# Optimization experiments

Measured on AMD Instinct MI355X. Metric: run time of the kernel, lower is better.

The kernel has to match this reference:

```python
import jax, jax.numpy as jnp
import numpy as np

N_IN = 16384
G = 64            # input grid resolution
K_UP = 8          # 2^3 children per voxel for kernel=2 stride=2 generative transpose conv
N_OUT = N_IN * K_UP
G2 = 2 * G        # output grid resolution
NUMS = 32768      # top-k prune budget
C = 64


def _np_coords_and_maps():
    """Build voxel coords, the 27-offset kernel map on upsampled coords, and a fake GT mask."""
    rng = np.random.default_rng(0)
    flat = rng.choice(G ** 3, size=N_IN, replace=False)
    c = np.stack(np.unravel_index(flat, (G, G, G)), axis=1).astype(np.int64)  # [N_IN,3]
    offs2 = np.stack(np.meshgrid(*([[0, 1]] * 3), indexing='ij'), -1).reshape(-1, 3)  # [8,3]
    cu = (2 * c[:, None, :] + offs2[None]).reshape(-1, 3)  # [N_OUT,3], order n*8+k
    lut = np.full(G2 ** 3, N_OUT, dtype=np.int64)
    key = (cu[:, 0] * G2 + cu[:, 1]) * G2 + cu[:, 2]
    lut[key] = np.arange(N_OUT)
    offs3 = np.stack(np.meshgrid(*([[-1, 0, 1]] * 3), indexing='ij'), -1).reshape(-1, 3)  # [27,3]
    nbr = np.empty((27, N_OUT), np.int64)
    for k, d in enumerate(offs3):
        q = cu + d
        valid = ((q >= 0) & (q < G2)).all(1)
        qk = np.where(valid, (q[:, 0] * G2 + q[:, 1]) * G2 + q[:, 2], 0)
        nbr[k] = np.where(valid, lut[qk], N_OUT)  # N_OUT = sentinel 'missing'
    gt = rng.random(N_OUT) < 0.3  # isin(out.C, ground_truth.C) membership mask
    return nbr.astype(np.int32), gt


def setup_inputs() -> dict:
    key = jax.random.key(0)
    ks = jax.random.split(key, 10)
    nbr, gt = _np_coords_and_maps()
    s = 0.05
    rn = lambda k, shape: jax.random.normal(k, shape, jnp.float32) * s
    z = lambda shape: jnp.zeros(shape, jnp.float32)
    return {
        "x_feats": jax.random.normal(ks[0], (N_IN, C), jnp.float32),
        "Wup": rn(ks[1], (K_UP, C, C)), "bup": z((C,)),
        "Wc0": rn(ks[2], (27, C, C)), "bc0": z((C,)),
        "W00": rn(ks[3], (3, 27, C, C // 4)), "b00": z((3, C // 4)),
        "W01": rn(ks[4], (3, 27, C // 4, C // 2)), "b01": z((3, C // 2)),
        "W10": rn(ks[5], (3, C, C // 4)), "b10": z((3, C // 4)),
        "W11": rn(ks[6], (3, 27, C // 4, C // 4)), "b11": z((3, C // 4)),
        "W12": rn(ks[7], (3, C // 4, C // 2)), "b12": z((3, C // 2)),
        "Wcls": rn(ks[8], (27, C, 1)), "bcls": z((1,)),
        "nbr_idx": jnp.asarray(nbr), "mask_true": jnp.asarray(gt),
        "nums": NUMS,
    }


def sparse_conv(feats, nbr, W, b):
    """Gather-GEMM-scatter sparse conv: feats [N,Cin], nbr [K,N] (N = missing), W [K,Cin,Cout]."""
    fp = jnp.concatenate([feats, jnp.zeros((1, feats.shape[1]), feats.dtype)], axis=0)
    def body(acc, wn):
        Wk, nk = wn
        return acc + fp[nk] @ Wk, None
    acc0 = jnp.zeros((feats.shape[0], W.shape[-1]), feats.dtype)
    out, _ = jax.lax.scan(body, acc0, (W, nbr))
    return out + b


def reference(x_feats, Wup, bup, Wc0, bc0, W00, b00, W01, b01, W10, b10, W11, b11, W12, b12, Wcls, bcls, nbr_idx, mask_true, nums):
    # generative transpose conv k=2 s=2: each voxel emits 8 children (no overlaps)
    up = jnp.einsum('nc,kcd->nkd', x_feats, Wup).reshape(-1, Wup.shape[-1]) + bup  # [N_OUT,C]
    out = jax.nn.relu(up)
    out = jax.nn.relu(sparse_conv(out, nbr_idx, Wc0, bc0))
    for i in range(3):  # 3 InceptionResNet blocks
        o0 = sparse_conv(jax.nn.relu(sparse_conv(out, nbr_idx, W00[i], b00[i])), nbr_idx, W01[i], b01[i])
        t = jax.nn.relu(out @ W10[i] + b10[i])            # 1x1 conv
        t = jax.nn.relu(sparse_conv(t, nbr_idx, W11[i], b11[i]))
        o1 = t @ W12[i] + b12[i]                          # 1x1 conv
        out = jnp.concatenate([o0, o1], axis=1) + out
    out_cls = sparse_conv(out, nbr_idx, Wcls, bcls)       # [N_OUT,1]
    _, idx = jax.lax.top_k(out_cls[:, 0], nums)           # istopk
    mask = jnp.zeros((out.shape[0],), bool).at[idx].set(True) | mask_true  # topk + isin(GT)
    pruned = out * mask[:, None].astype(out.dtype)        # pruning as mask (static shape)
    return out_cls, pruned, mask
```

## Files before the change

kernel.cpp:

```cpp
#include <hip/hip_runtime.h>
#include <cstdint>

#define NOUTC 131072
#define NINC  16384

using uint = unsigned int;

__device__ __forceinline__ uint fkey(float v){
  uint u = __float_as_uint(v);
  return (u & 0x80000000u) ? ~u : (u | 0x80000000u);
}

template<int ROWS, int CIN, int COUT, int TR, int TC, int NK, bool IDENT, bool RELU, bool RESID>
__global__ __launch_bounds__(256)
void spconv(const float* __restrict__ feats,
            const int*   __restrict__ nbr,
            const float* __restrict__ Wg,
            const float* __restrict__ bias,
            const float* __restrict__ resid,
            float*       __restrict__ outp,
            int ostride, int coff)
{
  static_assert(TR == 4, "TR must be 4");
  static_assert((ROWS / TR) * (COUT / TC) == 256, "thread tiling must cover 256 threads");
  constexpr int TPR = 256 / ROWS;
  static_assert(ROWS * TPR == 256, "");
  constexpr int GV = CIN / (4 * TPR);
  static_assert(CIN % (4 * TPR) == 0, "");
  constexpr int STR = ROWS + 4;

  __shared__ float Wl[CIN * COUT];
  __shared__ float ft[CIN][STR];

  const int t    = threadIdx.x;
  const int base = blockIdx.x * ROWS;

  constexpr int CT = COUT / TC;
  const int tcc = (t % CT) * TC;
  const int trr = (t / CT) * TR;

  const int gr    = t / TPR;
  const int gpart = t % TPR;

  float acc[TR][TC];
  #pragma unroll
  for (int a = 0; a < TR; ++a)
    #pragma unroll
    for (int b = 0; b < TC; ++b) acc[a][b] = 0.f;

  for (int k = 0; k < NK; ++k) {
    #pragma unroll
    for (int i = t; i < CIN * COUT; i += 256) Wl[i] = Wg[k * CIN * COUT + i];
    int gidx = IDENT ? (base + gr) : nbr[(size_t)k * NOUTC + base + gr];
    const float4* src = reinterpret_cast<const float4*>(feats + (size_t)gidx * CIN) + gpart * GV;
    #pragma unroll
    for (int j = 0; j < GV; ++j) {
      float4 v = src[j];
      int ci = (gpart * GV + j) * 4;
      ft[ci + 0][gr] = v.x; ft[ci + 1][gr] = v.y;
      ft[ci + 2][gr] = v.z; ft[ci + 3][gr] = v.w;
    }
    __syncthreads();
    #pragma unroll
    for (int ci = 0; ci < CIN; ++ci) {
      float4 f = *reinterpret_cast<const float4*>(&ft[ci][trr]);
      float fv[4] = {f.x, f.y, f.z, f.w};
      float wv[TC];
      if constexpr (TC == 4) {
        float4 w = *reinterpret_cast<const float4*>(&Wl[ci * COUT + tcc]);
        wv[0] = w.x; wv[1] = w.y; wv[2] = w.z; wv[3] = w.w;
      } else {
        float2 w = *reinterpret_cast<const float2*>(&Wl[ci * COUT + tcc]);
        wv[0] = w.x; wv[1] = w.y;
      }
      #pragma unroll
      for (int a = 0; a < TR; ++a)
        #pragma unroll
        for (int b = 0; b < TC; ++b)
          acc[a][b] = fmaf(fv[a], wv[b], acc[a][b]);
    }
    __syncthreads();
  }

  #pragma unroll
  for (int a = 0; a < TR; ++a) {
    int rr = base + trr + a;
    float o[TC];
    #pragma unroll
    for (int b = 0; b < TC; ++b) {
      float v = acc[a][b] + bias[tcc + b];
      if (RELU) v = v > 0.f ? v : 0.f;
      o[b] = v;
    }
    if (RESID) {
      #pragma unroll
      for (int b = 0; b < TC; ++b)
        o[b] += resid[(size_t)rr * 64 + coff + tcc + b];
    }
    float* dst = outp + (size_t)rr * ostride + coff + tcc;
    if constexpr (TC == 4) {
      float4 w4 = {o[0], o[1], o[2], o[3]};
      *reinterpret_cast<float4*>(dst) = w4;
    } else {
      float2 w2 = {o[0], o[1]};
      *reinterpret_cast<float2*>(dst) = w2;
    }
  }
}

__global__ __launch_bounds__(256)
void upsample_kernel(const float* __restrict__ x, const float* __restrict__ Wup,
                     const float* __restrict__ bup, float* __restrict__ outp)
{
  __shared__ float Wl[64 * 64];
  __shared__ float xt[64][68];
  const int t    = threadIdx.x;
  const int tile = blockIdx.x >> 3;
  const int k    = blockIdx.x & 7;
  const int base = tile * 64;

  #pragma unroll
  for (int i = t; i < 4096; i += 256) Wl[i] = Wup[k * 4096 + i];
  {
    const int gr = t >> 2, gp = t & 3;
    const float4* src = reinterpret_cast<const float4*>(x + (size_t)(base + gr) * 64) + gp * 4;
    #pragma unroll
    for (int j = 0; j < 4; ++j) {
      float4 v = src[j];
      int ci = (gp * 4 + j) * 4;
      xt[ci + 0][gr] = v.x; xt[ci + 1][gr] = v.y;
      xt[ci + 2][gr] = v.z; xt[ci + 3][gr] = v.w;
    }
  }
  __syncthreads();
  const int tcc = (t % 16) * 4, trr = (t / 16) * 4;
  float acc[4][4];
  #pragma unroll
  for (int a = 0; a < 4; ++a)
    #pragma unroll
    for (int b = 0; b < 4; ++b) acc[a][b] = 0.f;
  #pragma unroll
  for (int ci = 0; ci < 64; ++ci) {
    float4 f = *reinterpret_cast<const float4*>(&xt[ci][trr]);
    float4 w = *reinterpret_cast<const float4*>(&Wl[ci * 64 + tcc]);
    float fv[4] = {f.x, f.y, f.z, f.w};
    float wv[4] = {w.x, w.y, w.z, w.w};
    #pragma unroll
    for (int a = 0; a < 4; ++a)
      #pragma unroll
      for (int b = 0; b < 4; ++b) acc[a][b] = fmaf(fv[a], wv[b], acc[a][b]);
  }
  #pragma unroll
  for (int a = 0; a < 4; ++a) {
    int n = base + trr + a;
    float4 o;
    float v0 = acc[a][0] + bup[tcc + 0]; o.x = v0 > 0.f ? v0 : 0.f;
    float v1 = acc[a][1] + bup[tcc + 1]; o.y = v1 > 0.f ? v1 : 0.f;
    float v2 = acc[a][2] + bup[tcc + 2]; o.z = v2 > 0.f ? v2 : 0.f;
    float v3 = acc[a][3] + bup[tcc + 3]; o.w = v3 > 0.f ? v3 : 0.f;
    *reinterpret_cast<float4*>(outp + ((size_t)n * 8 + k) * 64 + tcc) = o;
  }
}

__global__ __launch_bounds__(256)
void cls_kernel(const float* __restrict__ feats, const int* __restrict__ nbr,
                const float* __restrict__ Wcls, const float* __restrict__ bcls,
                float* __restrict__ out_cls)
{
  const int wave = threadIdx.x >> 6;
  const int lane = threadIdx.x & 63;
  float wreg[27];
  #pragma unroll
  for (int k = 0; k < 27; ++k) wreg[k] = Wcls[k * 64 + lane];
  const int base = blockIdx.x * 32 + wave * 8;
  for (int rr = 0; rr < 8; ++rr) {
    const int n = base + rr;
    float s = 0.f;
    #pragma unroll
    for (int k = 0; k < 27; ++k) {
      int idx = nbr[(size_t)k * NOUTC + n];
      s = fmaf(feats[(size_t)idx * 64 + lane], wreg[k], s);
    }
    #pragma unroll
    for (int off = 32; off >= 1; off >>= 1) s += __shfl_xor(s, off, 64);
    if (lane == 0) out_cls[n] = s + bcls[0];
  }
}

__global__ void init_kernel(uint* hist1, uint* hist2, int* tie_cnt, int* flag,
                            float* fa, float* fb, float* t0, float* t1)
{
  int i = blockIdx.x * 256 + threadIdx.x;
  if (i < 65536) hist1[i] = 0;
  else if (i < 131072) hist2[i - 65536] = 0;
  if (i == 0) { tie_cnt[0] = 0; flag[0] = 0; }
  if (i < 64) { fa[(size_t)NOUTC * 64 + i] = 0.f; fb[(size_t)NOUTC * 64 + i] = 0.f; }
  if (i < 16) { t0[(size_t)NOUTC * 16 + i] = 0.f; t1[(size_t)NOUTC * 16 + i] = 0.f; }
}

__global__ void detect_kernel(const unsigned char* __restrict__ mt, int* flag)
{
  int i = blockIdx.x * 256 + threadIdx.x;
  int p = i * 4 + 1;
  if (p < NOUTC && mt[p] != 0) flag[0] = 1;
}

__global__ void hist1_kernel(const float* __restrict__ cls, uint* __restrict__ hist)
{
  for (int i = blockIdx.x * blockDim.x + threadIdx.x; i < NOUTC; i += gridDim.x * blockDim.x)
    atomicAdd(&hist[fkey(cls[i]) >> 16], 1u);
}

__global__ void scan1_kernel(const uint* __restrict__ hist, const int* __restrict__ nums,
                             uint* __restrict__ res)
{
  __shared__ uint chunk[256];
  const int t = threadIdx.x;
  uint s = 0;
  for (int j = 0; j < 256; ++j) s += hist[t * 256 + j];
  chunk[t] = s;
  __syncthreads();
  if (t == 0) {
    uint k = (uint)nums[0];
    uint cum = 0; int c = 255;
    for (; c > 0; --c) { if (cum + chunk[c] >= k) break; cum += chunk[c]; }
    int B = c * 256; uint cum2 = cum;
    for (int b = c * 256 + 255; b >= c * 256; --b) {
      if (cum2 + hist[b] >= k) { B = b; break; }
      cum2 += hist[b];
    }
    res[0] = (uint)B; res[1] = cum2;
  }
}

__global__ void hist2_kernel(const float* __restrict__ cls, const uint* __restrict__ res1,
                             uint* __restrict__ hist)
{
  const uint B = res1[0];
  for (int i = blockIdx.x * blockDim.x + threadIdx.x; i < NOUTC; i += gridDim.x * blockDim.x) {
    uint key = fkey(cls[i]);
    if ((key >> 16) == B) atomicAdd(&hist[key & 0xffffu], 1u);
  }
}

__global__ void scan2_kernel(const uint* __restrict__ hist, const uint* __restrict__ res1,
                             const int* __restrict__ nums, uint* __restrict__ res2)
{
  __shared__ uint chunk[256];
  const int t = threadIdx.x;
  uint s = 0;
  for (int j = 0; j < 256; ++j) s += hist[t * 256 + j];
  chunk[t] = s;
  __syncthreads();
  if (t == 0) {
    uint k = (uint)nums[0];
    uint cum = res1[1]; int c = 255;
    for (; c > 0; --c) { if (cum + chunk[c] >= k) break; cum += chunk[c]; }
    int L = c * 256; uint cum2 = cum;
    for (int b = c * 256 + 255; b >= c * 256; --b) {
      if (cum2 + hist[b] >= k) { L = b; break; }
      cum2 += hist[b];
    }
    res2[0] = (res1[0] << 16) | (uint)L;
    res2[1] = k - cum2;
  }
}

__global__ void mark_kernel(const float* __restrict__ cls, const uint* __restrict__ res2,
                            unsigned char* __restrict__ msel, int* tie_cnt, int* tie_idx)
{
  const uint T = res2[0];
  for (int i = blockIdx.x * blockDim.x + threadIdx.x; i < NOUTC; i += gridDim.x * blockDim.x) {
    uint key = fkey(cls[i]);
    msel[i] = key > T ? 1 : 0;
    if (key == T) {
      int p = atomicAdd(tie_cnt, 1);
      if (p < 4096) tie_idx[p] = i;
    }
  }
}

__global__ void tie_kernel(const uint* __restrict__ res2, const int* __restrict__ tie_cnt,
                           const int* __restrict__ tie_idx, unsigned char* __restrict__ msel)
{
  int need = (int)res2[1];
  int cnt = tie_cnt[0]; if (cnt > 4096) cnt = 4096;
  if (need <= 0) return;
  if (cnt <= need) {
    for (int i = threadIdx.x; i < cnt; i += 256) msel[tie_idx[i]] = 1;
  } else {
    for (int i = threadIdx.x; i < cnt; i += 256) {
      int my = tie_idx[i];
      int rank = 0;
      for (int j = 0; j < cnt; ++j) rank += (tie_idx[j] < my) ? 1 : 0;
      if (rank < need) msel[my] = 1;
    }
  }
}

__global__ void prune_kernel(const float* __restrict__ feats, const unsigned char* __restrict__ msel,
                             const void* __restrict__ mtrue, const int* __restrict__ flag,
                             float* __restrict__ dout)
{
  const unsigned char* mb = (const unsigned char*)mtrue;
  const int* mi = (const int*)mtrue;
  const bool bytes = (flag[0] != 0);
  float* pruned = dout + NOUTC;
  float* maskf  = dout + NOUTC + (size_t)NOUTC * 64;
  const float4* src = reinterpret_cast<const float4*>(feats);
  float4* dst = reinterpret_cast<float4*>(pruned);
  const int total = NOUTC * 16;
  for (int i = blockIdx.x * blockDim.x + threadIdx.x; i < total; i += gridDim.x * blockDim.x) {
    int n = i >> 4;
    bool mt = bytes ? (mb[n] != 0) : (mi[n] != 0);
    bool m = (msel[n] != 0) || mt;
    float4 v = src[i];
    float4 z = {0.f, 0.f, 0.f, 0.f};
    dst[i] = m ? v : z;
    if ((i & 15) == 0) maskf[n] = m ? 1.f : 0.f;
  }
}

extern "C" void kernel_launch(void* const* d_in, const int* in_sizes, int n_in,
                              void* d_out, int out_size, void* d_ws, size_t ws_size,
                              hipStream_t stream)
{
  const float* x    = (const float*)d_in[0];
  const float* Wup  = (const float*)d_in[1];
  const float* bup  = (const float*)d_in[2];
  const float* Wc0  = (const float*)d_in[3];
  const float* bc0  = (const float*)d_in[4];
  const float* W00  = (const float*)d_in[5];
  const float* b00  = (const float*)d_in[6];
  const float* W01  = (const float*)d_in[7];
  const float* b01  = (const float*)d_in[8];
  const float* W10  = (const float*)d_in[9];
  const float* b10  = (const float*)d_in[10];
  const float* W11  = (const float*)d_in[11];
  const float* b11  = (const float*)d_in[12];
  const float* W12  = (const float*)d_in[13];
  const float* b12  = (const float*)d_in[14];
  const float* Wcls = (const float*)d_in[15];
  const float* bcls = (const float*)d_in[16];
  const int*   nbr  = (const int*)d_in[17];
  const void*  mtrue= d_in[18];
  const int*   nums = (const int*)d_in[19];

  float* dout = (float*)d_out;

  float* fa = (float*)d_ws;
  float* t0 = fa + (size_t)(NOUTC + 1) * 64;
  float* t1 = t0 + (size_t)(NOUTC + 1) * 16;
  uint*  hist1 = (uint*)(t1 + (size_t)(NOUTC + 1) * 16);
  uint*  hist2 = hist1 + 65536;
  uint*  res1  = hist2 + 65536;
  uint*  res2  = res1 + 2;
  int*   tie_cnt = (int*)(res2 + 2);
  int*   flag    = tie_cnt + 1;
  int*   tie_idx = flag + 1;
  unsigned char* msel = (unsigned char*)(tie_idx + 4096);
  float* fb = dout + NOUTC;

  init_kernel<<<512, 256, 0, stream>>>(hist1, hist2, tie_cnt, flag, fa, fb, t0, t1);
  detect_kernel<<<128, 256, 0, stream>>>((const unsigned char*)mtrue, flag);

  upsample_kernel<<<2048, 256, 0, stream>>>(x, Wup, bup, fa);
  spconv<64, 64, 64, 4, 4, 27, false, true, false>
      <<<NOUTC / 64, 256, 0, stream>>>(fa, nbr, Wc0, bc0, nullptr, fb, 64, 0);

  const float* cur = fb; float* nxt = fa;
  for (int i = 0; i < 3; ++i) {
    spconv<128, 64, 16, 4, 2, 27, false, true, false>
        <<<NOUTC / 128, 256, 0, stream>>>(cur, nbr, W00 + (size_t)i * 27 * 64 * 16,
                                          b00 + i * 16, nullptr, t0, 16, 0);
    spconv<128, 16, 32, 4, 4, 27, false, false, true>
        <<<NOUTC / 128, 256, 0, stream>>>(t0, nbr, W01 + (size_t)i * 27 * 16 * 32,
                                          b01 + i * 32, cur, nxt, 64, 0);
    spconv<128, 64, 16, 4, 2, 1, true, true, false>
        <<<NOUTC / 128, 256, 0, stream>>>(cur, nullptr, W10 + (size_t)i * 64 * 16,
                                          b10 + i * 16, nullptr, t1, 16, 0);
    spconv<128, 16, 16, 4, 2, 27, false, true, false>
        <<<NOUTC / 128, 256, 0, stream>>>(t1, nbr, W11 + (size_t)i * 27 * 16 * 16,
                                          b11 + i * 16, nullptr, t0, 16, 0);
    spconv<128, 16, 32, 4, 4, 1, true, false, true>
        <<<NOUTC / 128, 256, 0, stream>>>(t0, nullptr, W12 + (size_t)i * 16 * 32,
                                          b12 + i * 32, cur, nxt, 64, 32);
    float* tmp = (float*)cur; cur = nxt; nxt = tmp;
  }

  cls_kernel<<<NOUTC / 32, 256, 0, stream>>>(cur, nbr, Wcls, bcls, dout);

  hist1_kernel<<<512, 256, 0, stream>>>(dout, hist1);
  scan1_kernel<<<1, 256, 0, stream>>>(hist1, nums, res1);
  hist2_kernel<<<512, 256, 0, stream>>>(dout, res1, hist2);
  scan2_kernel<<<1, 256, 0, stream>>>(hist2, res1, nums, res2);
  mark_kernel<<<512, 256, 0, stream>>>(dout, res2, msel, tie_cnt, tie_idx);
  tie_kernel<<<1, 256, 0, stream>>>(res2, tie_cnt, tie_idx, msel);
  prune_kernel<<<4096, 256, 0, stream>>>(cur, msel, mtrue, flag, dout);
}
```

Measured before the change: 1.547 ms.

## Rewrite sparse conv with 8x8 register tiles, split-K reduction and register prefetch

Replaces the spconv kernel with spconv2, where each thread computes an 8x8 output tile and the input-channel loop is split across threads, with a shared-memory tree reduction at the end. The next kernel offset's gathered features and weights are prefetched into registers while the current offset is being computed. The weight tile in LDS is padded to cut bank conflicts. This raises arithmetic intensity per LDS load and hides gather latency, at the cost of more registers (64 accumulators plus staging buffers), possible occupancy loss, and extra reduction synchronisation.

```diff
diff --git a/kernel.cpp b/kernel.cpp
--- a/kernel.cpp
+++ b/kernel.cpp
@@ -11,99 +11,154 @@
   return (u & 0x80000000u) ? ~u : (u | 0x80000000u);
 }
 
-template<int ROWS, int CIN, int COUT, int TR, int TC, int NK, bool IDENT, bool RELU, bool RESID>
-__global__ __launch_bounds__(256)
-void spconv(const float* __restrict__ feats,
-            const int*   __restrict__ nbr,
-            const float* __restrict__ Wg,
-            const float* __restrict__ bias,
-            const float* __restrict__ resid,
-            float*       __restrict__ outp,
-            int ostride, int coff)
-{
-  static_assert(TR == 4, "TR must be 4");
-  static_assert((ROWS / TR) * (COUT / TC) == 256, "thread tiling must cover 256 threads");
-  constexpr int TPR = 256 / ROWS;
-  static_assert(ROWS * TPR == 256, "");
-  constexpr int GV = CIN / (4 * TPR);
-  static_assert(CIN % (4 * TPR) == 0, "");
-  constexpr int STR = ROWS + 4;
-
-  __shared__ float Wl[CIN * COUT];
-  __shared__ float ft[CIN][STR];
+template<int ROWS, int CIN, int COUT, int SPLIT, int THREADS, int NK,
+         bool IDENT, bool RELU, bool RESID>
+__global__ __launch_bounds__(THREADS)
+void spconv2(const float* __restrict__ feats, const int* __restrict__ nbr,
+             const float* __restrict__ Wg, const float* __restrict__ bias,
+             const float* __restrict__ resid, float* __restrict__ outp,
+             int ostride, int coff)
+{
+  constexpr int RG = ROWS / 8, CG = COUT / 8;
+  static_assert(RG * CG * SPLIT == THREADS, "bad thread tiling");
+  constexpr int CIPT = CIN / SPLIT;
+  static_assert(CIPT * SPLIT == CIN, "");
+  constexpr int STR  = ROWS + 4;
+  constexpr int WSTR = COUT + 4;
+  constexpr int TPR  = THREADS / ROWS;
+  static_assert(TPR * ROWS == THREADS, "");
+  constexpr int FSTG = CIN / TPR;
+  static_assert(FSTG % 4 == 0, "");
+  constexpr int WSTG = (CIN * COUT) / THREADS;
+  constexpr int NSLOT = THREADS / SPLIT;
+
+  constexpr int MAIN_FL = CIN * STR + CIN * WSTR;
+  constexpr int RED_FL  = (SPLIT > 1) ? (THREADS / 2) * 64 : 0;
+  constexpr int LDS_FL  = MAIN_FL > RED_FL ? MAIN_FL : RED_FL;
+  __shared__ float smem[LDS_FL];
+  float* ft = smem;
+  float* Wl = smem + CIN * STR;
 
   const int t    = threadIdx.x;
   const int base = blockIdx.x * ROWS;
-
-  constexpr int CT = COUT / TC;
-  const int tcc = (t % CT) * TC;
-  const int trr = (t / CT) * TR;
-
-  const int gr    = t / TPR;
-  const int gpart = t % TPR;
-
-  float acc[TR][TC];
-  #pragma unroll
-  for (int a = 0; a < TR; ++a)
-    #pragma unroll
-    for (int b = 0; b < TC; ++b) acc[a][b] = 0.f;
+  const int sp   = t % SPLIT;
+  const int slot = t / SPLIT;
+  const int rg = slot / CG, cg = slot % CG;
+  const int trr = rg * 8, tcc = cg * 8;
+  const int gr = t / TPR, part = t % TPR;
+
+  float4 fstg[FSTG / 4];
+  alignas(16) float wstg[WSTG];
+  float acc[8][8];
+  #pragma unroll
+  for (int a = 0; a < 8; ++a)
+    #pragma unroll
+    for (int b = 0; b < 8; ++b) acc[a][b] = 0.f;
+
+  auto load_f = [&](int k) {
+    int gidx = IDENT ? (base + gr) : nbr[(size_t)k * NOUTC + base + gr];
+    const float4* src = reinterpret_cast<const float4*>(feats + (size_t)gidx * CIN + part * FSTG);
+    #pragma unroll
+    for (int j = 0; j < FSTG / 4; ++j) fstg[j] = src[j];
+  };
+  auto load_w = [&](int k) {
+    const float* wsrc = Wg + (size_t)k * CIN * COUT + t * WSTG;
+    if constexpr (WSTG % 4 == 0) {
+      #pragma unroll
+      for (int m = 0; m < WSTG / 4; ++m)
+        *reinterpret_cast<float4*>(&wstg[4 * m]) = reinterpret_cast<const float4*>(wsrc)[m];
+    } else {
+      *reinterpret_cast<float2*>(&wstg[0]) = *reinterpret_cast<const float2*>(wsrc);
+    }
+  };
+
+  load_f(0); load_w(0);
 
   for (int k = 0; k < NK; ++k) {
     #pragma unroll
-    for (int i = t; i < CIN * COUT; i += 256) Wl[i] = Wg[k * CIN * COUT + i];
-    int gidx = IDENT ? (base + gr) : nbr[(size_t)k * NOUTC + base + gr];
-    const float4* src = reinterpret_cast<const float4*>(feats + (size_t)gidx * CIN) + gpart * GV;
-    #pragma unroll
-    for (int j = 0; j < GV; ++j) {
-      float4 v = src[j];
-      int ci = (gpart * GV + j) * 4;
-      ft[ci + 0][gr] = v.x; ft[ci + 1][gr] = v.y;
-      ft[ci + 2][gr] = v.z; ft[ci + 3][gr] = v.w;
+    for (int j = 0; j < FSTG / 4; ++j) {
+      int ci = part * FSTG + 4 * j;
+      ft[(ci + 0) * STR + gr] = fstg[j].x;
+      ft[(ci + 1) * STR + gr] = fstg[j].y;
+      ft[(ci + 2) * STR + gr] = fstg[j].z;
+      ft[(ci + 3) * STR + gr] = fstg[j].w;
+    }
+    #pragma unroll
+    for (int m = 0; m < WSTG; ++m) {
+      int widx = t * WSTG + m;
+      Wl[(widx / COUT) * WSTR + (widx % COUT)] = wstg[m];
     }
     __syncthreads();
-    #pragma unroll
-    for (int ci = 0; ci < CIN; ++ci) {
-      float4 f = *reinterpret_cast<const float4*>(&ft[ci][trr]);
-      float fv[4] = {f.x, f.y, f.z, f.w};
-      float wv[TC];
-      if constexpr (TC == 4) {
-        float4 w = *reinterpret_cast<const float4*>(&Wl[ci * COUT + tcc]);
-        wv[0] = w.x; wv[1] = w.y; wv[2] = w.z; wv[3] = w.w;
-      } else {
-        float2 w = *reinterpret_cast<const float2*>(&Wl[ci * COUT + tcc]);
-        wv[0] = w.x; wv[1] = w.y;
+    if (k + 1 < NK) { load_f(k + 1); load_w(k + 1); }
+    #pragma unroll 4
+    for (int i = 0; i < CIPT; ++i) {
+      int ci = sp + SPLIT * i;
+      float4 f0 = *reinterpret_cast<const float4*>(&ft[ci * STR + trr]);
+      float4 f1 = *reinterpret_cast<const float4*>(&ft[ci * STR + trr + 4]);
+      float4 w0 = *reinterpret_cast<const float4*>(&Wl[ci * WSTR + tcc]);
+      float4 w1 = *reinterpret_cast<const float4*>(&Wl[ci * WSTR + tcc + 4]);
+      float fv[8] = {f0.x, f0.y, f0.z, f0.w, f1.x, f1.y, f1.z, f1.w};
+      float wv[8] = {w0.x, w0.y, w0.z, w0.w, w1.x, w1.y, w1.z, w1.w};
+      #pragma unroll
+      for (int a = 0; a < 8; ++a)
+        #pragma unroll
+        for (int b = 0; b < 8; ++b)
+          acc[a][b] = fmaf(fv[a], wv[b], acc[a][b]);
+    }
+    __syncthreads();
+  }
+
+  if constexpr (SPLIT > 1) {
+    float* red = smem;
+    for (int off = SPLIT / 2; off >= 1; off >>= 1) {
+      __syncthreads();
+      if (sp >= off && sp < 2 * off) {
+        float* dst = red + ((size_t)((sp - off) * NSLOT + slot)) * 64;
+        #pragma unroll
+        for (int a = 0; a < 8; ++a) {
+          float4 v0 = {acc[a][0], acc[a][1], acc[a][2], acc[a][3]};
+          float4 v1 = {acc[a][4], acc[a][5], acc[a][6], acc[a][7]};
+          *reinterpret_cast<float4*>(dst + a * 8)     = v0;
+          *reinterpret_cast<float4*>(dst + a * 8 + 4) = v1;
+        }
       }
+      __syncthreads();
+      if (sp < off) {
+        const float* s = red + ((size_t)(sp * NSLOT + slot)) * 64;
+        #pragma unroll
+        for (int a = 0; a < 8; ++a) {
+          float4 v0 = *reinterpret_cast<const float4*>(s + a * 8);
+          float4 v1 = *reinterpret_cast<const float4*>(s + a * 8 + 4);
+          acc[a][0] += v0.x; acc[a][1] += v0.y; acc[a][2] += v0.z; acc[a][3] += v0.w;
+          acc[a][4] += v1.x; acc[a][5] += v1.y; acc[a][6] += v1.z; acc[a][7] += v1.w;
+        }
+      }
+    }
+  }
+
+  if (sp == 0) {
+    #pragma unroll
+    for (int a = 0; a < 8; ++a) {
+      int r = base + trr + a;
+      float o[8];
       #pragma unroll
-      for (int a = 0; a < TR; ++a)
-        #pragma unroll
-        for (int b = 0; b < TC; ++b)
-          acc[a][b] = fmaf(fv[a], wv[b], acc[a][b]);
-    }
-    __syncthreads();
-  }
-
-  #pragma unroll
-  for (int a = 0; a < TR; ++a) {
-    int rr = base + trr + a;
-    float o[TC];
-    #pragma unroll
-    for (int b = 0; b < TC; ++b) {
-      float v = acc[a][b] + bias[tcc + b];
-      if (RELU) v = v > 0.f ? v : 0.f;
-      o[b] = v;
-    }
-    if (RESID) {
-      #pragma unroll
-      for (int b = 0; b < TC; ++b)
-        o[b] += resid[(size_t)rr * 64 + coff + tcc + b];
-    }
-    float* dst = outp + (size_t)rr * ostride + coff + tcc;
-    if constexpr (TC == 4) {
-      float4 w4 = {o[0], o[1], o[2], o[3]};
-      *reinterpret_cast<float4*>(dst) = w4;
-    } else {
-      float2 w2 = {o[0], o[1]};
-      *reinterpret_cast<float2*>(dst) = w2;
+      for (int b = 0; b < 8; ++b) {
+        float v = acc[a][b] + bias[tcc + b];
+        if (RELU) v = v > 0.f ? v : 0.f;
+        o[b] = v;
+      }
+      if (RESID) {
+        const float* rs = resid + (size_t)r * 64 + coff + tcc;
+        float4 r0 = *reinterpret_cast<const float4*>(rs);
+        float4 r1 = *reinterpret_cast<const float4*>(rs + 4);
+        o[0] += r0.x; o[1] += r0.y; o[2] += r0.z; o[3] += r0.w;
+        o[4] += r1.x; o[5] += r1.y; o[6] += r1.z; o[7] += r1.w;
+      }
+      float* dst = outp + (size_t)r * ostride + coff + tcc;
+      float4 s0 = {o[0], o[1], o[2], o[3]};
+      float4 s1 = {o[4], o[5], o[6], o[7]};
+      *reinterpret_cast<float4*>(dst)     = s0;
+      *reinterpret_cast<float4*>(dst + 4) = s1;
     }
   }
 }
@@ -365,24 +420,25 @@
   detect_kernel<<<128, 256, 0, stream>>>((const unsigned char*)mtrue, flag);
 
   upsample_kernel<<<2048, 256, 0, stream>>>(x, Wup, bup, fa);
-  spconv<64, 64, 64, 4, 4, 27, false, true, false>
-      <<<NOUTC / 64, 256, 0, stream>>>(fa, nbr, Wc0, bc0, nullptr, fb, 64, 0);
+
+  spconv2<128, 64, 64, 2, 256, 27, false, true, false>
+      <<<NOUTC / 128, 256, 0, stream>>>(fa, nbr, Wc0, bc0, nullptr, fb, 64, 0);
 
   const float* cur = fb; float* nxt = fa;
   for (int i = 0; i < 3; ++i) {
-    spconv<128, 64, 16, 4, 2, 27, false, true, false>
-        <<<NOUTC / 128, 256, 0, stream>>>(cur, nbr, W00 + (size_t)i * 27 * 64 * 16,
+    spconv2<128, 64, 16, 4, 128, 27, false, true, false>
+        <<<NOUTC / 128, 128, 0, stream>>>(cur, nbr, W00 + (size_t)i * 27 * 64 * 16,
                                           b00 + i * 16, nullptr, t0, 16, 0);
-    spconv<128, 16, 32, 4, 4, 27, false, false, true>
+    spconv2<128, 16, 32, 4, 256, 27, false, false, true>
         <<<NOUTC / 128, 256, 0, stream>>>(t0, nbr, W01 + (size_t)i * 27 * 16 * 32,
                                           b01 + i * 32, cur, nxt, 64, 0);
-    spconv<128, 64, 16, 4, 2, 1, true, true, false>
-        <<<NOUTC / 128, 256, 0, stream>>>(cur, nullptr, W10 + (size_t)i * 64 * 16,
+    spconv2<128, 64, 16, 4, 128, 1, true, true, false>
+        <<<NOUTC / 128, 128, 0, stream>>>(cur, nullptr, W10 + (size_t)i * 64 * 16,
                                           b10 + i * 16, nullptr, t1, 16, 0);
-    spconv<128, 16, 16, 4, 2, 27, false, true, false>
-        <<<NOUTC / 128, 256, 0, stream>>>(t1, nbr, W11 + (size_t)i * 27 * 16 * 16,
+    spconv2<128, 16, 16, 4, 128, 27, false, true, false>
+        <<<NOUTC / 128, 128, 0, stream>>>(t1, nbr, W11 + (size_t)i * 27 * 16 * 16,
                                           b11 + i * 16, nullptr, t0, 16, 0);
-    spconv<128, 16, 32, 4, 4, 1, true, false, true>
+    spconv2<128, 16, 32, 4, 256, 1, true, false, true>
         <<<NOUTC / 128, 256, 0, stream>>>(t0, nullptr, W12 + (size_t)i * 16 * 32,
                                           b12 + i * 32, cur, nxt, 64, 32);
     float* tmp = (float*)cur; cur = nxt; nxt = tmp;
```

Result: faster. 1.297 ms (-16.1%).
